# Performance work log

Hardware: AMD Instinct MI355X
Metric: run time of the kernel (lower is better)

## Reference

```python
import jax, jax.numpy as jnp
import numpy as np
from jax import lax

EPS = 1e-5

def _rsign(x, beta):
    # per-channel learnable shift followed by sign binarization
    return jnp.sign(x + beta[None, :, None, None])

def _scaled_sign_conv(x, w, stride, pad):
    # XNOR-style binarized weights: sign(W) * mean(|W|) per output filter
    alpha = jnp.mean(jnp.abs(w), axis=(1, 2, 3), keepdims=True)
    wb = jnp.sign(w) * alpha
    return lax.conv_general_dilated(x, wb, (stride, stride), [(pad, pad), (pad, pad)],
                                    dimension_numbers=('NCHW', 'OIHW', 'NCHW'))

def _bn(x, gamma, beta):
    # training-mode batch norm (batch statistics), matching torch default forward
    m = jnp.mean(x, axis=(0, 2, 3), keepdims=True)
    v = jnp.var(x, axis=(0, 2, 3), keepdims=True)
    xn = (x - m) * lax.rsqrt(v + EPS)
    return xn * gamma[None, :, None, None] + beta[None, :, None, None]

def _rprelu(x, gamma, zeta, slope):
    g = gamma[None, :, None, None]
    s = slope[None, :, None, None]
    xs = x - g
    return jnp.where(xs > 0, xs, s * xs) + zeta[None, :, None, None]

def _avgpool2(x):
    B, C, H, W = x.shape
    return x.reshape(B, C, H // 2, 2, W // 2, 2).mean(axis=(3, 5))

def reference(x, rsign1_beta, w1, bn1_gamma, bn1_beta, rsign2_beta, w2, bn2_gamma, bn2_beta, pr_gamma, pr_zeta, pr_slope):
    # layer1: RSign -> 3x3 stride-2 scaled_sign conv -> BN
    out1 = _bn(_scaled_sign_conv(_rsign(x, rsign1_beta), w1, 2, 1), bn1_gamma, bn1_beta)
    out1 = out1 + _avgpool2(x)
    out1 = _rprelu(out1, pr_gamma, pr_zeta, pr_slope)
    # layer2 (shared weights, called twice with identical inputs -> identical outputs)
    out2 = _bn(_scaled_sign_conv(_rsign(out1, rsign2_beta), w2, 1, 0), bn2_gamma, bn2_beta)
    y = out2 + out1
    return jnp.concatenate([y, y], axis=1)

def setup_inputs() -> dict:
    key = jax.random.key(0)
    ks = jax.random.split(key, 8)
    B, C, H, W = 32, 256, 56, 56
    return {
        'x': jax.random.normal(ks[0], (B, C, H, W), jnp.float32),
        'rsign1_beta': jax.random.normal(ks[1], (C,), jnp.float32) * 0.1,
        'w1': jax.random.normal(ks[2], (C, C, 3, 3), jnp.float32) * 0.05,
        'bn1_gamma': jnp.ones((C,), jnp.float32),
        'bn1_beta': jnp.zeros((C,), jnp.float32),
        'rsign2_beta': jax.random.normal(ks[3], (C,), jnp.float32) * 0.1,
        'w2': jax.random.normal(ks[4], (C, C, 1, 1), jnp.float32) * 0.05,
        'bn2_gamma': jnp.ones((C,), jnp.float32),
        'bn2_beta': jnp.zeros((C,), jnp.float32),
        'pr_gamma': jax.random.normal(ks[5], (C,), jnp.float32) * 0.1,
        'pr_zeta': jax.random.normal(ks[6], (C,), jnp.float32) * 0.1,
        'pr_slope': jnp.full((C,), 0.25, jnp.float32),
    }
```

## Files before the change

kernel.cpp:

```cpp
#include <hip/hip_runtime.h>
#include <stdint.h>

typedef unsigned long long u64;
typedef uint32_t u32;

#define BB  32
#define CC  256
#define HH  56
#define WW  56
#define OHH 28
#define OWW 28
#define NPIX (BB*OHH*OWW)

__global__ __launch_bounds__(256) void rrb_prep_w(const float* __restrict__ w1,
                                                  const float* __restrict__ w2,
                                                  u32* __restrict__ wp1, u32* __restrict__ wp2,
                                                  float* __restrict__ alpha1, float* __restrict__ alpha2,
                                                  u32* __restrict__ stats_zero) {
    __shared__ float red[256];
    int co = blockIdx.x & 255;
    int t = threadIdx.x;
    int wid = t >> 6, lane = t & 63;
    if (blockIdx.x == 0) {
        #pragma unroll
        for (int k = 0; k < 6; ++k) stats_zero[k * 256 + t] = 0u;
    }
    float asum = 0.f;
    if (blockIdx.x < 256) {
        const float* wr = w1 + (size_t)co * 2304 + (size_t)t * 9;
        float v[9];
        #pragma unroll
        for (int k = 0; k < 9; ++k) { v[k] = wr[k]; asum += fabsf(v[k]); }
        #pragma unroll
        for (int k = 0; k < 9; ++k) {
            u64 m = __ballot(v[k] > 0.f);
            if (lane == 0)
                *(u64*)&wp1[((size_t)co * 9 + k) * 8 + 2 * wid] = m;
        }
    } else {
        float v = w2[co * 256 + t];
        asum = fabsf(v);
        u64 m = __ballot(v > 0.f);
        if (lane == 0) *(u64*)&wp2[co * 8 + 2 * wid] = m;
    }
    red[t] = asum; __syncthreads();
    for (int st = 128; st > 0; st >>= 1) {
        if (t < st) red[t] += red[t + st];
        __syncthreads();
    }
    if (t == 0) {
        if (blockIdx.x < 256) alpha1[co] = red[0] / 2304.f;
        else                  alpha2[co] = red[0] / 256.f;
    }
}

__global__ __launch_bounds__(256) void rrb_pack_x(const float* __restrict__ x,
                                                  const float* __restrict__ rsb1,
                                                  u32* __restrict__ xb, float* __restrict__ pool) {
    int i = blockIdx.x * 256 + threadIdx.x;
    int s  = i & 3;
    int i2 = i >> 2;
    int ow = i2 % OWW;
    int i3 = i2 / OWW;
    int oh = i3 % OHH;
    int i4 = i3 / OHH;
    int n  = i4 & 31;
    int j  = i4 >> 5;
    int c0 = 32 * j + 8 * s;
    const float* base = x + (((size_t)(n * CC + c0) * HH + 2 * oh) * WW + 2 * ow);

    float2 a0[8], a1[8];
    #pragma unroll
    for (int cc = 0; cc < 8; ++cc) {
        const float* p = base + (size_t)cc * (HH * WW);
        a0[cc] = *(const float2*)p;
        a1[cc] = *(const float2*)(p + WW);
    }
    float4 b0 = *(const float4*)&rsb1[c0];
    float4 b1 = *(const float4*)&rsb1[c0 + 4];

    u32 w00 = 0, w01 = 0, w10 = 0, w11 = 0;
    float pv[8];
    #pragma unroll
    for (int cc = 0; cc < 8; ++cc) {
        float b = (cc < 4) ? ((const float*)&b0)[cc] : ((const float*)&b1)[cc - 4];
        w00 |= (u32)(a0[cc].x + b > 0.f) << cc;
        w01 |= (u32)(a0[cc].y + b > 0.f) << cc;
        w10 |= (u32)(a1[cc].x + b > 0.f) << cc;
        w11 |= (u32)(a1[cc].y + b > 0.f) << cc;
        pv[cc] = (a0[cc].x + a0[cc].y + a1[cc].x + a1[cc].y) * 0.25f;
    }
    w00 <<= 8 * s; w01 <<= 8 * s; w10 <<= 8 * s; w11 <<= 8 * s;
    w00 |= __shfl_xor(w00, 1); w00 |= __shfl_xor(w00, 2);
    w01 |= __shfl_xor(w01, 1); w01 |= __shfl_xor(w01, 2);
    w10 |= __shfl_xor(w10, 1); w10 |= __shfl_xor(w10, 2);
    w11 |= __shfl_xor(w11, 1); w11 |= __shfl_xor(w11, 2);

    float* pp = pool + ((size_t)(n * OHH + oh) * OWW + ow) * CC + c0;
    *(float4*)&pp[0] = make_float4(pv[0], pv[1], pv[2], pv[3]);
    *(float4*)&pp[4] = make_float4(pv[4], pv[5], pv[6], pv[7]);

    u32* xo = xb + (((size_t)(n * HH + 2 * oh) * WW + 2 * ow) * 8) + j;
    u32 wsel = (s == 0) ? w00 : (s == 1) ? w01 : (s == 2) ? w10 : w11;
    int off = (s == 0) ? 0 : (s == 1) ? 8 : (s == 2) ? WW * 8 : WW * 8 + 8;
    xo[off] = wsel;
}

__global__ __launch_bounds__(256) void rrb_conv1(const u32* __restrict__ xb,
                                                 const u32* __restrict__ wp1,
                                                 short* __restrict__ S1,
                                                 int* __restrict__ s_sum, u64* __restrict__ s_sq) {
    __shared__ u32 xs[3 * WW * 8];
    int blk = blockIdx.x;
    int n = blk / OHH, oh = blk - n * OHH;
    int t = threadIdx.x;
    int r0 = 2 * oh - 1;
    for (int i = t; i < 3 * WW * 8; i += 256) {
        int row = i / (WW * 8);
        int ih = r0 + row;
        xs[i] = (ih >= 0) ? xb[((size_t)(n * HH + ih) * WW) * 8 + (i - row * WW * 8)] : 0u;
    }
    u32 wreg[72];
    {
        const u32* wsrc = wp1 + (size_t)t * 72;
        #pragma unroll
        for (int i = 0; i < 72; ++i) wreg[i] = wsrc[i];
    }
    __syncthreads();
    bool oh0 = (oh == 0);
    int bsum = 0; long long bsq = 0;
    short* outp = S1 + ((size_t)(n * OHH + oh) * OWW) * CC + t;
    for (int ow = 0; ow < OWW; ++ow) {
        int S = 0;
        #pragma unroll
        for (int kh = 0; kh < 3; ++kh) {
            bool vkh = !(kh == 0 && oh0);
            #pragma unroll
            for (int kw = 0; kw < 3; ++kw) {
                int iw = 2 * ow + kw - 1;
                bool ok = vkh && (iw >= 0);
                int iwc = iw < 0 ? 0 : iw;
                const u32* xp = &xs[(kh * WW + iwc) * 8];
                int p = 0;
                #pragma unroll
                for (int j = 0; j < 8; ++j) p += __popc(xp[j] ^ wreg[(kh * 3 + kw) * 8 + j]);
                S += ok ? (256 - 2 * p) : 0;
            }
        }
        outp[ow * CC] = (short)S;
        bsum += S;
        bsq += (long long)S * S;
    }
    atomicAdd(&s_sum[t], bsum);
    atomicAdd(&s_sq[t], (u64)bsq);
}

__device__ __forceinline__ void bn_fold(const int* ssum, const u64* ssq,
                                        const float* alpha, const float* gamma,
                                        const float* beta, int c, float& a, float& b) {
    const double N = (double)NPIX;
    double s = (double)ssum[c];
    double q = (double)ssq[c];
    double mS = s / N;
    double vS = q / N - mS * mS;
    double al = (double)alpha[c];
    double scale = (double)gamma[c] / sqrt(al * al * vS + 1e-5);
    a = (float)(al * scale);
    b = (float)((double)beta[c] - al * mS * scale);
}

__global__ __launch_bounds__(256) void rrb_out1(const short* __restrict__ S1,
                                                float* __restrict__ pool,
                                                const int* __restrict__ ssum, const u64* __restrict__ ssq,
                                                const float* __restrict__ alpha1,
                                                const float* __restrict__ bn1g, const float* __restrict__ bn1b,
                                                const float* __restrict__ pg, const float* __restrict__ pz,
                                                const float* __restrict__ ps, const float* __restrict__ rsb2,
                                                u32* __restrict__ x2b) {
    int blk = blockIdx.x;
    int half = blk & 1;
    int rest = blk >> 1;
    int n = rest / OHH, oh = rest - n * OHH;
    int owlo = half * 14;
    int c = threadIdx.x;
    int wid = c >> 6, lane = c & 63;
    float a, b;
    bn_fold(ssum, ssq, alpha1, bn1g, bn1b, c, a, b);
    float g = pg[c], z = pz[c], s = ps[c], b2 = rsb2[c];
    size_t pixbase = ((size_t)(n * OHH + oh) * OWW + owlo);
    const short* sp = S1 + pixbase * CC + c;
    float* pp = pool + pixbase * CC + c;
    u32* xo = x2b + pixbase * 8;
    float sv[14], pv[14];
    #pragma unroll
    for (int k = 0; k < 14; ++k) sv[k] = (float)sp[k * CC];
    #pragma unroll
    for (int k = 0; k < 14; ++k) pv[k] = pp[k * CC];
    #pragma unroll
    for (int k = 0; k < 14; ++k) {
        float v = a * sv[k] + b + pv[k];
        float xsv = v - g;
        float o = (xsv > 0.f ? xsv : s * xsv) + z;
        pp[k * CC] = o;
        u64 m = __ballot(o + b2 > 0.f);
        if (lane == 0) *(u64*)&xo[k * 8 + 2 * wid] = m;
    }
}

__global__ __launch_bounds__(256) void rrb_conv2(const u32* __restrict__ x2b,
                                                 const u32* __restrict__ wp2,
                                                 short* __restrict__ S2,
                                                 int* __restrict__ s_sum, u64* __restrict__ s_sq) {
    __shared__ u32 xs[14 * 8];
    int blk = blockIdx.x;
    int half = blk & 1;
    int rest = blk >> 1;
    int n = rest / OHH, oh = rest - n * OHH;
    int owlo = half * 14;
    int t = threadIdx.x;
    size_t pixbase = ((size_t)(n * OHH + oh) * OWW + owlo);
    const u32* src = x2b + pixbase * 8;
    if (t < 14 * 8) xs[t] = src[t];
    u32 wr[8];
    {
        const u32* wsv = wp2 + (size_t)t * 8;
        #pragma unroll
        for (int j = 0; j < 8; ++j) wr[j] = wsv[j];
    }
    __syncthreads();
    int bsum = 0; long long bsq = 0;
    short* outp = S2 + pixbase * CC + t;
    #pragma unroll
    for (int ow = 0; ow < 14; ++ow) {
        int p = 0;
        #pragma unroll
        for (int j = 0; j < 8; ++j) p += __popc(xs[ow * 8 + j] ^ wr[j]);
        int S = 256 - 2 * p;
        outp[ow * CC] = (short)S;
        bsum += S;
        bsq += (long long)S * S;
    }
    atomicAdd(&s_sum[t], bsum);
    atomicAdd(&s_sq[t], (u64)bsq);
}

__global__ __launch_bounds__(256) void rrb_final(const short* __restrict__ S2,
                                                 const float* __restrict__ out1,
                                                 const int* __restrict__ ssum, const u64* __restrict__ ssq,
                                                 const float* __restrict__ alpha2,
                                                 const float* __restrict__ bn2g, const float* __restrict__ bn2b,
                                                 float* __restrict__ y) {
    __shared__ float lds[256 * 29];
    int blk = blockIdx.x;
    int n = blk / OHH, oh = blk - n * OHH;
    int c = threadIdx.x;
    float a, b;
    bn_fold(ssum, ssq, alpha2, bn2g, bn2b, c, a, b);
    size_t pixbase = ((size_t)(n * OHH + oh) * OWW);
    const short* sp = S2 + pixbase * CC + c;
    const float* op = out1 + pixbase * CC + c;
    #pragma unroll
    for (int ow = 0; ow < OWW; ++ow)
        lds[c * 29 + ow] = a * (float)sp[ow * CC] + b + op[ow * CC];
    __syncthreads();
    #pragma unroll
    for (int it = 0; it < 7; ++it) {
        int idx = it * 256 + c;
        int cp = idx / 7, qq = idx - cp * 7;
        const float* lp = &lds[cp * 29 + 4 * qq];
        float4 v = make_float4(lp[0], lp[1], lp[2], lp[3]);
        float* dst = y + ((size_t)(n * 2 * CC + cp) * OHH + oh) * OWW + 4 * qq;
        *(float4*)dst = v;
        *(float4*)(dst + (size_t)CC * OHH * OWW) = v;
    }
}

extern "C" void kernel_launch(void* const* d_in, const int* in_sizes, int n_in,
                              void* d_out, int out_size, void* d_ws, size_t ws_size,
                              hipStream_t stream) {
    const float* x    = (const float*)d_in[0];
    const float* rsb1 = (const float*)d_in[1];
    const float* w1   = (const float*)d_in[2];
    const float* bn1g = (const float*)d_in[3];
    const float* bn1b = (const float*)d_in[4];
    const float* rsb2 = (const float*)d_in[5];
    const float* w2   = (const float*)d_in[6];
    const float* bn2g = (const float*)d_in[7];
    const float* bn2b = (const float*)d_in[8];
    const float* pg   = (const float*)d_in[9];
    const float* pz   = (const float*)d_in[10];
    const float* ps   = (const float*)d_in[11];
    float* y = (float*)d_out;

    char* ws = (char*)d_ws;
    if (ws_size < 55488512) return;

    u32*   wp1    = (u32*)(ws + 0);
    u32*   wp2    = (u32*)(ws + 73728);
    float* alpha1 = (float*)(ws + 81920);
    float* alpha2 = (float*)(ws + 82944);
    int*   st1_sum = (int*)(ws + 88064);
    u64*   st1_sq  = (u64*)(ws + 89088);
    int*   st2_sum = (int*)(ws + 91136);
    u64*   st2_sq  = (u64*)(ws + 92160);
    u32*   xb   = (u32*)(ws + 94208);
    float* pool = (float*)(ws + 3305472);
    short* S1   = (short*)(ws + 28995584);
    u32*   x2b  = (u32*)(ws + 41840640);
    short* S2   = (short*)(ws + 42643456);

    rrb_prep_w<<<512, 256, 0, stream>>>(w1, w2, wp1, wp2, alpha1, alpha2,
                                        (u32*)(ws + 88064));
    rrb_pack_x<<<(BB * OHH * OWW * 8 * 4) / 256, 256, 0, stream>>>(x, rsb1, xb, pool);
    rrb_conv1<<<BB * OHH, 256, 0, stream>>>(xb, wp1, S1, st1_sum, st1_sq);
    rrb_out1<<<BB * OHH * 2, 256, 0, stream>>>(S1, pool, st1_sum, st1_sq, alpha1,
                                               bn1g, bn1b, pg, pz, ps, rsb2, x2b);
    rrb_conv2<<<BB * OHH * 2, 256, 0, stream>>>(x2b, wp2, S2, st2_sum, st2_sq);
    rrb_final<<<BB * OHH, 256, 0, stream>>>(S2, pool, st2_sum, st2_sq, alpha2,
                                            bn2g, bn2b, y);
}
```

Measured before the change: 157.6 us.

## Fuse conv2 stats into out1 and recompute conv2 in final kernel

Merges the out1 and conv2 kernels so the binarized layer-2 input stays in shared memory and only the BN2 statistics are accumulated there. The final kernel re-derives the sign bits from out1, recomputes the cheap popcount 1x1 conv, and applies BN2 and the residual directly. This drops the x2b and S2 global buffers and one kernel launch, removing their writes and reads. In exchange the popcount conv runs twice and the final kernel holds more registers and more shared memory.

```diff
diff --git a/kernel.cpp b/kernel.cpp
--- a/kernel.cpp
+++ b/kernel.cpp
@@ -169,14 +169,16 @@
     b = (float)((double)beta[c] - al * mS * scale);
 }
 
-__global__ __launch_bounds__(256) void rrb_out1(const short* __restrict__ S1,
-                                                float* __restrict__ pool,
-                                                const int* __restrict__ ssum, const u64* __restrict__ ssq,
-                                                const float* __restrict__ alpha1,
-                                                const float* __restrict__ bn1g, const float* __restrict__ bn1b,
-                                                const float* __restrict__ pg, const float* __restrict__ pz,
-                                                const float* __restrict__ ps, const float* __restrict__ rsb2,
-                                                u32* __restrict__ x2b) {
+__global__ __launch_bounds__(256) void rrb_out1c2(const short* __restrict__ S1,
+                                                  float* __restrict__ pool,
+                                                  const int* __restrict__ ssum, const u64* __restrict__ ssq,
+                                                  const float* __restrict__ alpha1,
+                                                  const float* __restrict__ bn1g, const float* __restrict__ bn1b,
+                                                  const float* __restrict__ pg, const float* __restrict__ pz,
+                                                  const float* __restrict__ ps, const float* __restrict__ rsb2,
+                                                  const u32* __restrict__ wp2,
+                                                  int* __restrict__ s_sum2, u64* __restrict__ s_sq2) {
+    __shared__ u32 xs[14 * 8];
     int blk = blockIdx.x;
     int half = blk & 1;
     int rest = blk >> 1;
@@ -190,7 +192,6 @@
     size_t pixbase = ((size_t)(n * OHH + oh) * OWW + owlo);
     const short* sp = S1 + pixbase * CC + c;
     float* pp = pool + pixbase * CC + c;
-    u32* xo = x2b + pixbase * 8;
     float sv[14], pv[14];
     #pragma unroll
     for (int k = 0; k < 14; ++k) sv[k] = (float)sp[k * CC];
@@ -203,65 +204,70 @@
         float o = (xsv > 0.f ? xsv : s * xsv) + z;
         pp[k * CC] = o;
         u64 m = __ballot(o + b2 > 0.f);
-        if (lane == 0) *(u64*)&xo[k * 8 + 2 * wid] = m;
-    }
-}
-
-__global__ __launch_bounds__(256) void rrb_conv2(const u32* __restrict__ x2b,
-                                                 const u32* __restrict__ wp2,
-                                                 short* __restrict__ S2,
-                                                 int* __restrict__ s_sum, u64* __restrict__ s_sq) {
-    __shared__ u32 xs[14 * 8];
-    int blk = blockIdx.x;
-    int half = blk & 1;
-    int rest = blk >> 1;
-    int n = rest / OHH, oh = rest - n * OHH;
-    int owlo = half * 14;
-    int t = threadIdx.x;
-    size_t pixbase = ((size_t)(n * OHH + oh) * OWW + owlo);
-    const u32* src = x2b + pixbase * 8;
-    if (t < 14 * 8) xs[t] = src[t];
+        if (lane == 0) *(u64*)&xs[k * 8 + 2 * wid] = m;
+    }
+    __syncthreads();
     u32 wr[8];
     {
-        const u32* wsv = wp2 + (size_t)t * 8;
+        const u32* wsv = wp2 + (size_t)c * 8;
         #pragma unroll
         for (int j = 0; j < 8; ++j) wr[j] = wsv[j];
     }
-    __syncthreads();
     int bsum = 0; long long bsq = 0;
-    short* outp = S2 + pixbase * CC + t;
-    #pragma unroll
-    for (int ow = 0; ow < 14; ++ow) {
+    #pragma unroll
+    for (int k = 0; k < 14; ++k) {
         int p = 0;
         #pragma unroll
-        for (int j = 0; j < 8; ++j) p += __popc(xs[ow * 8 + j] ^ wr[j]);
+        for (int j = 0; j < 8; ++j) p += __popc(xs[k * 8 + j] ^ wr[j]);
         int S = 256 - 2 * p;
-        outp[ow * CC] = (short)S;
         bsum += S;
         bsq += (long long)S * S;
     }
-    atomicAdd(&s_sum[t], bsum);
-    atomicAdd(&s_sq[t], (u64)bsq);
-}
-
-__global__ __launch_bounds__(256) void rrb_final(const short* __restrict__ S2,
-                                                 const float* __restrict__ out1,
+    atomicAdd(&s_sum2[c], bsum);
+    atomicAdd(&s_sq2[c], (u64)bsq);
+}
+
+__global__ __launch_bounds__(256) void rrb_final(const float* __restrict__ out1,
                                                  const int* __restrict__ ssum, const u64* __restrict__ ssq,
                                                  const float* __restrict__ alpha2,
                                                  const float* __restrict__ bn2g, const float* __restrict__ bn2b,
+                                                 const float* __restrict__ rsb2,
+                                                 const u32* __restrict__ wp2,
                                                  float* __restrict__ y) {
+    __shared__ u32 xs[OWW * 8];
     __shared__ float lds[256 * 29];
     int blk = blockIdx.x;
     int n = blk / OHH, oh = blk - n * OHH;
     int c = threadIdx.x;
+    int wid = c >> 6, lane = c & 63;
     float a, b;
     bn_fold(ssum, ssq, alpha2, bn2g, bn2b, c, a, b);
+    float b2 = rsb2[c];
     size_t pixbase = ((size_t)(n * OHH + oh) * OWW);
-    const short* sp = S2 + pixbase * CC + c;
     const float* op = out1 + pixbase * CC + c;
-    #pragma unroll
-    for (int ow = 0; ow < OWW; ++ow)
-        lds[c * 29 + ow] = a * (float)sp[ow * CC] + b + op[ow * CC];
+    float ov[OWW];
+    #pragma unroll
+    for (int ow = 0; ow < OWW; ++ow) ov[ow] = op[ow * CC];
+    #pragma unroll
+    for (int ow = 0; ow < OWW; ++ow) {
+        u64 m = __ballot(ov[ow] + b2 > 0.f);
+        if (lane == 0) *(u64*)&xs[ow * 8 + 2 * wid] = m;
+    }
+    u32 wr[8];
+    {
+        const u32* wsv = wp2 + (size_t)c * 8;
+        #pragma unroll
+        for (int j = 0; j < 8; ++j) wr[j] = wsv[j];
+    }
+    __syncthreads();
+    #pragma unroll
+    for (int ow = 0; ow < OWW; ++ow) {
+        int p = 0;
+        #pragma unroll
+        for (int j = 0; j < 8; ++j) p += __popc(xs[ow * 8 + j] ^ wr[j]);
+        int S = 256 - 2 * p;
+        lds[c * 29 + ow] = a * (float)S + b + ov[ow];
+    }
     __syncthreads();
     #pragma unroll
     for (int it = 0; it < 7; ++it) {
@@ -293,7 +299,7 @@
     float* y = (float*)d_out;
 
     char* ws = (char*)d_ws;
-    if (ws_size < 55488512) return;
+    if (ws_size < 41840640) return;
 
     u32*   wp1    = (u32*)(ws + 0);
     u32*   wp2    = (u32*)(ws + 73728);
@@ -306,16 +312,14 @@
     u32*   xb   = (u32*)(ws + 94208);
     float* pool = (float*)(ws + 3305472);
     short* S1   = (short*)(ws + 28995584);
-    u32*   x2b  = (u32*)(ws + 41840640);
-    short* S2   = (short*)(ws + 42643456);
 
     rrb_prep_w<<<512, 256, 0, stream>>>(w1, w2, wp1, wp2, alpha1, alpha2,
                                         (u32*)(ws + 88064));
     rrb_pack_x<<<(BB * OHH * OWW * 8 * 4) / 256, 256, 0, stream>>>(x, rsb1, xb, pool);
     rrb_conv1<<<BB * OHH, 256, 0, stream>>>(xb, wp1, S1, st1_sum, st1_sq);
-    rrb_out1<<<BB * OHH * 2, 256, 0, stream>>>(S1, pool, st1_sum, st1_sq, alpha1,
-                                               bn1g, bn1b, pg, pz, ps, rsb2, x2b);
-    rrb_conv2<<<BB * OHH * 2, 256, 0, stream>>>(x2b, wp2, S2, st2_sum, st2_sq);
-    rrb_final<<<BB * OHH, 256, 0, stream>>>(S2, pool, st2_sum, st2_sq, alpha2,
-                                            bn2g, bn2b, y);
-}
+    rrb_out1c2<<<BB * OHH * 2, 256, 0, stream>>>(S1, pool, st1_sum, st1_sq, alpha1,
+                                                 bn1g, bn1b, pg, pz, ps, rsb2,
+                                                 wp2, st2_sum, st2_sq);
+    rrb_final<<<BB * OHH, 256, 0, stream>>>(pool, st2_sum, st2_sq, alpha2,
+                                            bn2g, bn2b, rsb2, wp2, y);
+}
```

Result: faster. 149.6 us (-5.1%).
